# Optimization experiments

Hardware: AMD Instinct MI355X
Metric: run time of the kernel (lower is better)

Reference implementation:

```python
import jax, jax.numpy as jnp
import numpy as np
import math

FILT_LEN = 10  # all Farras / dual filters are 10-tap
INV_SQRT2 = 1.0 / math.sqrt(2.0)

# Farras first-stage analysis filters (fs_farras), shape [tree(2), lo/hi(2), 10]
_F = 0.08838834764832
_G = 0.01122679215254
_H = 0.69587998903400
FAF_NP = np.array([
    [[0.0, -_F, _F, _H, _H, _F, -_F, _G, _G, 0.0],
     [0.0, -_G, _G, _F, _F, -_H, _H, -_F, -_F, 0.0]],
    [[_G, _G, -_F, _F, _H, _H, _F, -_F, 0.0, 0.0],
     [0.0, 0.0, -_F, -_F, _H, -_H, _F, _F, _G, -_G]]], dtype=np.float32)
# Kingsbury Q-shift dual filters (duelfilt / dualfilt1), shape [tree(2), lo/hi(2), 10]
_A = 0.03516384
_B = 0.08832942
_C = 0.23389032
_D = 0.76027237
_E = 0.58751830
_K = 0.11430184
AF_NP = np.array([
    [[_A, 0.0, -_B, _C, _D, _E, 0.0, -_K, 0.0, 0.0],
     [0.0, 0.0, -_K, 0.0, _E, -_D, _C, _B, 0.0, -_A]],
    [[0.0, 0.0, -_K, 0.0, _E, _D, _C, -_B, 0.0, _A],
     [-_A, 0.0, _B, _C, -_D, _E, 0.0, -_K, 0.0, 0.0]]], dtype=np.float32)


def _afb_axis(x, lo_f, hi_f, axis):
    """1D circular analysis filter bank along spatial `axis` (1=rows, 2=cols).
    x: (B,H,W,C). Returns (lo, hi), each halved along `axis`.
    Math: x <- cshift(x,-L); y = downsample2(fullconv(x,f)); wrap-add first L taps.
    """
    N = x.shape[axis]
    L = FILT_LEN // 2
    C = x.shape[-1]
    x = jnp.roll(x, -L, axis=axis)

    def conv(f):
        kf = f[::-1].astype(x.dtype)  # lax does correlation -> flip for convolution
        if axis == 1:
            ker = jnp.tile(kf.reshape(FILT_LEN, 1, 1, 1), (1, 1, 1, C))
            pad = [(FILT_LEN - 1, FILT_LEN - 1), (0, 0)]
            strides = (2, 1)
        else:
            ker = jnp.tile(kf.reshape(1, FILT_LEN, 1, 1), (1, 1, 1, C))
            pad = [(0, 0), (FILT_LEN - 1, FILT_LEN - 1)]
            strides = (1, 2)
        return jax.lax.conv_general_dilated(
            x, ker, window_strides=strides, padding=pad,
            dimension_numbers=('NHWC', 'HWIO', 'NHWC'),
            feature_group_count=C)  # depthwise, per-channel identical filter

    def wrap(y):
        # y has N//2 + L samples along axis; fold periodic tail into head
        head = (jax.lax.slice_in_dim(y, 0, L, axis=axis)
                + jax.lax.slice_in_dim(y, N // 2, N // 2 + L, axis=axis))
        body = jax.lax.slice_in_dim(y, L, N // 2, axis=axis)
        return jnp.concatenate([head, body], axis=axis)

    return wrap(conv(lo_f)), wrap(conv(hi_f))


def afb2d(x, lo_row, hi_row, lo_col, hi_col):
    """2D separable analysis filter bank: returns (lo, [lohi, hilo, hihi])."""
    Lr, Hr = _afb_axis(x, lo_row, hi_row, axis=1)
    lo, w0 = _afb_axis(Lr, lo_col, hi_col, axis=2)
    w1, w2 = _afb_axis(Hr, lo_col, hi_col, axis=2)
    return lo, [w0, w1, w2]


def _add_sub(a, b):
    return (a + b) * INV_SQRT2, (a - b) * INV_SQRT2


def _dtcwt(x, Faf, af, level):
    x = x / 2
    w = [[[None, None] for _ in range(2)] for _ in range(level + 1)]
    for m in range(2):
        for n in range(2):
            lo, w[0][m][n] = afb2d(x, Faf[m, 0], Faf[m, 1], Faf[n, 0], Faf[n, 1])
            for j in range(1, level):
                lo, w[j][m][n] = afb2d(lo, af[m, 0], af[m, 1], af[n, 0], af[n, 1])
            w[level][m][n] = lo
    # combine dual trees into (approx) complex pairs
    for j in range(level):
        for s in range(3):
            w[j][0][0][s], w[j][1][1][s] = _add_sub(w[j][0][0][s], w[j][1][1][s])
            w[j][0][1][s], w[j][1][0][s] = _add_sub(w[j][0][1][s], w[j][1][0][s])
    # multiscale 2x2 tiling reassembly (concat=True path)
    wc = w
    for j in range(level - 1, 0, -1):
        for a in range(2):
            for b in range(2):
                wc[j][a][b] = jnp.concatenate([
                    jnp.concatenate([wc[j + 1][a][b], wc[j][a][b][0]], axis=2),
                    jnp.concatenate([wc[j][a][b][1], wc[j][a][b][2]], axis=2)], axis=1)
    tiles = []
    for a in range(2):
        for b in range(2):
            tiles.append(jnp.concatenate([
                jnp.concatenate([wc[1][a][b], wc[0][a][b][0]], axis=2),
                jnp.concatenate([wc[0][a][b][1], wc[0][a][b][2]], axis=2)], axis=1))
    w0, w1, w2, w3 = tiles
    return jnp.concatenate([jnp.concatenate([w0, w1], axis=2),
                            jnp.concatenate([w2, w3], axis=2)], axis=1)


def setup_inputs() -> dict:
    key = jax.random.key(0)
    x = jax.random.normal(key, (8, 512, 512, 3), dtype=jnp.float32)
    return {"x": x, "Faf": jnp.asarray(FAF_NP), "af": jnp.asarray(AF_NP), "level": 3}


def reference(x, Faf, af, level):
    return _dtcwt(x, Faf, af, int(level))
```

## Files before the change

### kernel.cpp

```cpp
#include <hip/hip_runtime.h>


#define FF 0.08838834764832f
#define GG 0.01122679215254f
#define HHc 0.69587998903400f
#define AAc 0.03516384f
#define BBc 0.08832942f
#define CCc 0.23389032f
#define DDc 0.76027237f
#define EEc 0.58751830f
#define KKc 0.11430184f

__device__ __constant__ float c_filt[2][2][2][10] = {
  {
    { {0.f,-FF, FF, HHc, HHc, FF,-FF, GG, GG, 0.f},
      {0.f,-GG, GG, FF, FF,-HHc, HHc,-FF,-FF, 0.f} },
    { {GG, GG,-FF, FF, HHc, HHc, FF,-FF, 0.f, 0.f},
      {0.f, 0.f,-FF,-FF, HHc,-HHc, FF, FF, GG,-GG} }
  },
  {
    { {AAc, 0.f,-BBc, CCc, DDc, EEc, 0.f,-KKc, 0.f, 0.f},
      {0.f, 0.f,-KKc, 0.f, EEc,-DDc, CCc, BBc, 0.f,-AAc} },
    { {0.f, 0.f,-KKc, 0.f, EEc, DDc, CCc,-BBc, 0.f, AAc},
      {-AAc, 0.f, BBc, CCc,-DDc, EEc, 0.f,-KKc, 0.f, 0.f} }
  }
};

__device__ __forceinline__ void cmb(float& a, float& b) {
  const float k = 0.70710678118654752440f;
  const float s = (a + b) * k, d = (a - b) * k;
  a = s; b = d;
}

__device__ __forceinline__ int swz4(int f4) { return f4 ^ ((f4 >> 3) & 7); }

template<int LVL, int N, int Ho, int Wo, int NT>
__global__ __launch_bounds__(NT) void fused_level(
    const float* __restrict__ src,
    float* __restrict__ llout,
    float* __restrict__ out)
{
  constexpr int half = N / 2;
  constexpr int W2 = 2 * Wo + 8;
  constexpr int NF = (LVL == 0) ? 4 : 8;
  constexpr int ROWF = 3 * N;
  constexpr int FL = 3 * W2;
  constexpr int SIF4 = (3 * W2 * NF) / 4 + 4;
  constexpr size_t ZS = (size_t)8 * N * N * 3;
  constexpr size_t ZOUT = (size_t)8 * half * half * 3;
  static_assert(Ho * Wo * 2 == NT, "stage-B thread map (z-pair split)");
  __shared__ __align__(16) float inter[Ho * SIF4 * 4];

  const int jt = blockIdx.x, it = blockIdx.y, b = blockIdx.z;
  const int i0 = it * Ho, j0 = jt * Wo;
  const int tid = threadIdx.x;

  int base = (2 * j0 - 4) * 3;
  if (base < 0) base += ROWF;

  constexpr int I4 = FL / 4;
  for (int item = tid; item < Ho * I4; item += NT) {
    const int il = item / I4;
    const int q4 = (item - il * I4) * 4;
    int fg = base + q4;
    if (fg >= ROWF) fg -= ROWF;
    const int ig = i0 + il;
    float acc[NF][4];
#pragma unroll
    for (int f = 0; f < NF; ++f)
#pragma unroll
      for (int k = 0; k < 4; ++k) acc[f][k] = 0.f;

    if constexpr (LVL == 0) {
      const float* sp = src + (size_t)b * N * ROWF + fg;
#pragma unroll
      for (int t = 0; t < 10; ++t) {
        const int r = (2 * ig + 5 - t) & (N - 1);
        const float4 v = *(const float4*)(sp + (size_t)r * ROWF);
#pragma unroll
        for (int f = 0; f < 4; ++f) {
          const float fc = c_filt[0][f >> 1][f & 1][t];
          acc[f][0] += fc * v.x; acc[f][1] += fc * v.y;
          acc[f][2] += fc * v.z; acc[f][3] += fc * v.w;
        }
      }
#pragma unroll
      for (int f = 0; f < 4; ++f)
#pragma unroll
        for (int k = 0; k < 4; ++k) acc[f][k] *= 0.5f;
    } else {
#pragma unroll
      for (int z = 0; z < 4; ++z) {
        const int m = z >> 1;
        const float* sp = src + (size_t)z * ZS + (size_t)b * N * ROWF + fg;
#pragma unroll
        for (int t = 0; t < 10; ++t) {
          const int r = (2 * ig + 5 - t) & (N - 1);
          const float4 v = *(const float4*)(sp + (size_t)r * ROWF);
          const float fl = c_filt[1][m][0][t], fh = c_filt[1][m][1][t];
          acc[2 * z][0] += fl * v.x; acc[2 * z][1] += fl * v.y;
          acc[2 * z][2] += fl * v.z; acc[2 * z][3] += fl * v.w;
          acc[2 * z + 1][0] += fh * v.x; acc[2 * z + 1][1] += fh * v.y;
          acc[2 * z + 1][2] += fh * v.z; acc[2 * z + 1][3] += fh * v.w;
        }
      }
    }
#pragma unroll
    for (int k = 0; k < 4; ++k) {
      const int fq = q4 + k;
      if constexpr (NF == 4) {
        float4 w = make_float4(acc[0][k], acc[1][k], acc[2][k], acc[3][k]);
        *(float4*)&inter[(il * SIF4 + swz4(fq)) * 4] = w;
      } else {
        float4 w0 = make_float4(acc[0][k], acc[1][k], acc[2][k], acc[3][k]);
        float4 w1 = make_float4(acc[4][k], acc[5][k], acc[6][k], acc[7][k]);
        *(float4*)&inter[(il * SIF4 + swz4(2 * fq)) * 4] = w0;
        *(float4*)&inter[(il * SIF4 + swz4(2 * fq + 1)) * 4] = w1;
      }
    }
  }
  __syncthreads();

  {
    const int pr = (tid >= Ho * Wo) ? 1 : 0;
    const int t7 = tid - pr * Ho * Wo;
    const int il = t7 / Wo, jl = t7 - (t7 / Wo) * Wo;
    const int za = pr, zb = 3 - pr;
    float LLa[3] = {}, LHa[3] = {}, HLa[3] = {}, HHa[3] = {};
    float LLb[3] = {}, LHb[3] = {}, HLb[3] = {}, HHb[3] = {};
#pragma unroll
    for (int s = 0; s < 10; ++s) {
      const int wl = 2 * jl + 9 - s;
      constexpr int BK = (LVL == 0) ? 0 : 1;
      const float fla = c_filt[BK][pr][0][s],     fha = c_filt[BK][pr][1][s];
      const float flb = c_filt[BK][1 - pr][0][s], fhb = c_filt[BK][1 - pr][1][s];
#pragma unroll
      for (int c = 0; c < 3; ++c) {
        float aa, da, ab, db;
        if constexpr (LVL == 0) {
          const int f4 = wl * 3 + c;
          const float4 v = *(const float4*)&inter[(il * SIF4 + swz4(f4)) * 4];
          aa = v.x; da = v.y; ab = v.z; db = v.w;
        } else {
          const int f4 = (wl * 3 + c) * 2;
          const float4 v0 = *(const float4*)&inter[(il * SIF4 + swz4(f4)) * 4];
          const float4 v1 = *(const float4*)&inter[(il * SIF4 + swz4(f4 + 1)) * 4];
          aa = pr ? v0.z : v0.x; da = pr ? v0.w : v0.y;
          ab = pr ? v1.x : v1.z; db = pr ? v1.y : v1.w;
        }
        LLa[c] += fla * aa; LHa[c] += fha * aa;
        HLa[c] += fla * da; HHa[c] += fha * da;
        LLb[c] += flb * ab; LHb[c] += fhb * ab;
        HLb[c] += flb * db; HHb[c] += fhb * db;
      }
    }
#pragma unroll
    for (int c = 0; c < 3; ++c) {
      cmb(LHa[c], LHb[c]); cmb(HLa[c], HLb[c]); cmb(HHa[c], HHb[c]);
    }
    const int ig = i0 + il, jg = j0 + jl;
    const size_t outB = (size_t)b * (1024u * 1024u * 3u);
    {
      const int m = za >> 1, n = za & 1;
      const int r0 = m * 512, c0 = n * 512;
      float* pLL;
      if constexpr (LVL == 2)
        pLL = out + outB + ((size_t)(r0 + ig) * 1024 + (c0 + jg)) * 3;
      else
        pLL = llout + (size_t)za * ZOUT + (((size_t)b * half + ig) * half + jg) * 3;
      pLL[0] = LLa[0]; pLL[1] = LLa[1]; pLL[2] = LLa[2];
      float* pLH = out + outB + ((size_t)(r0 + ig) * 1024 + (c0 + half + jg)) * 3;
      pLH[0] = LHa[0]; pLH[1] = LHa[1]; pLH[2] = LHa[2];
      float* pHL = out + outB + ((size_t)(r0 + half + ig) * 1024 + (c0 + jg)) * 3;
      pHL[0] = HLa[0]; pHL[1] = HLa[1]; pHL[2] = HLa[2];
      float* pHH = out + outB + ((size_t)(r0 + half + ig) * 1024 + (c0 + half + jg)) * 3;
      pHH[0] = HHa[0]; pHH[1] = HHa[1]; pHH[2] = HHa[2];
    }
    {
      const int m = zb >> 1, n = zb & 1;
      const int r0 = m * 512, c0 = n * 512;
      float* pLL;
      if constexpr (LVL == 2)
        pLL = out + outB + ((size_t)(r0 + ig) * 1024 + (c0 + jg)) * 3;
      else
        pLL = llout + (size_t)zb * ZOUT + (((size_t)b * half + ig) * half + jg) * 3;
      pLL[0] = LLb[0]; pLL[1] = LLb[1]; pLL[2] = LLb[2];
      float* pLH = out + outB + ((size_t)(r0 + ig) * 1024 + (c0 + half + jg)) * 3;
      pLH[0] = LHb[0]; pLH[1] = LHb[1]; pLH[2] = LHb[2];
      float* pHL = out + outB + ((size_t)(r0 + half + ig) * 1024 + (c0 + jg)) * 3;
      pHL[0] = HLb[0]; pHL[1] = HLb[1]; pHL[2] = HLb[2];
      float* pHH = out + outB + ((size_t)(r0 + half + ig) * 1024 + (c0 + half + jg)) * 3;
      pHH[0] = HHb[0]; pHH[1] = HHb[1]; pHH[2] = HHb[2];
    }
  }
}

extern "C" void kernel_launch(void* const* d_in, const int* in_sizes, int n_in,
                              void* d_out, int out_size, void* d_ws, size_t ws_size,
                              hipStream_t stream) {
  (void)in_sizes; (void)n_in; (void)out_size; (void)ws_size;
  const float* x = (const float*)d_in[0];
  float* out = (float*)d_out;
  float* LL1 = (float*)d_ws;
  float* LL2 = LL1 + 6291456;

  fused_level<0, 512, 4, 32, 256><<<dim3(8, 64, 8), 256, 0, stream>>>(x, LL1, out);
  fused_level<1, 256, 8, 16, 256><<<dim3(8, 16, 8), 256, 0, stream>>>(LL1, LL2, out);
  fused_level<2, 128, 4, 16, 128><<<dim3(4, 16, 8), 128, 0, stream>>>(LL2, nullptr, out);
}
```

Measured before the change: 175.3 us.

## Stage level-0 input rows in shared memory and enlarge level-2 tiles

Level 0 gets its own kernel that first loads the block's 2*Ho+8 input rows into shared memory with coalesced float4 loads. The vertical 10-tap filter then reads from LDS, so it no longer issues ten overlapping global row loads per output. The generic kernel drops its level-0 branches, and the level-2 launch moves from 4x16 tiles with 128 threads to 8x16 tiles with 256 threads. The cost is extra shared memory per block at level 0, which may lower occupancy.

```diff
diff --git a/kernel.cpp b/kernel.cpp
--- a/kernel.cpp
+++ b/kernel.cpp
@@ -34,6 +34,130 @@
 
 __device__ __forceinline__ int swz4(int f4) { return f4 ^ ((f4 >> 3) & 7); }
 
+template<int N, int Ho, int Wo, int NT>
+__global__ __launch_bounds__(NT) void fused_level0(
+    const float* __restrict__ src,
+    float* __restrict__ llout,
+    float* __restrict__ out)
+{
+  constexpr int half = N / 2;
+  constexpr int W2 = 2 * Wo + 8;
+  constexpr int ROWF = 3 * N;
+  constexpr int FL = 3 * W2;
+  constexpr int I4 = FL / 4;
+  constexpr int RR = 2 * Ho + 8;
+  constexpr int SIF4 = 3 * W2 + 4;
+  constexpr size_t ZOUT = (size_t)8 * half * half * 3;
+  static_assert(Ho * Wo * 2 == NT, "stage-B thread map (z-pair split)");
+  __shared__ __align__(16) float raw[RR * FL];
+  __shared__ __align__(16) float inter[Ho * SIF4 * 4];
+
+  const int jt = blockIdx.x, it = blockIdx.y, b = blockIdx.z;
+  const int i0 = it * Ho, j0 = jt * Wo;
+  const int tid = threadIdx.x;
+
+  int base = (2 * j0 - 4) * 3;
+  if (base < 0) base += ROWF;
+
+  const float* sb = src + (size_t)b * N * ROWF;
+  for (int item = tid; item < RR * I4; item += NT) {
+    const int lr = item / I4;
+    const int q4 = (item - lr * I4) * 4;
+    int fg = base + q4;
+    if (fg >= ROWF) fg -= ROWF;
+    const int g = (2 * i0 - 4 + lr) & (N - 1);
+    *(float4*)&raw[lr * FL + q4] = *(const float4*)(sb + (size_t)g * ROWF + fg);
+  }
+  __syncthreads();
+
+  for (int item = tid; item < Ho * I4; item += NT) {
+    const int il = item / I4;
+    const int q4 = (item - il * I4) * 4;
+    float acc[4][4];
+#pragma unroll
+    for (int f = 0; f < 4; ++f)
+#pragma unroll
+      for (int k = 0; k < 4; ++k) acc[f][k] = 0.f;
+#pragma unroll
+    for (int t = 0; t < 10; ++t) {
+      const int lr = 2 * il + 9 - t;
+      const float4 v = *(const float4*)&raw[lr * FL + q4];
+#pragma unroll
+      for (int f = 0; f < 4; ++f) {
+        const float fc = c_filt[0][f >> 1][f & 1][t];
+        acc[f][0] += fc * v.x; acc[f][1] += fc * v.y;
+        acc[f][2] += fc * v.z; acc[f][3] += fc * v.w;
+      }
+    }
+#pragma unroll
+    for (int f = 0; f < 4; ++f)
+#pragma unroll
+      for (int k = 0; k < 4; ++k) acc[f][k] *= 0.5f;
+#pragma unroll
+    for (int k = 0; k < 4; ++k) {
+      const int fq = q4 + k;
+      float4 w = make_float4(acc[0][k], acc[1][k], acc[2][k], acc[3][k]);
+      *(float4*)&inter[(il * SIF4 + swz4(fq)) * 4] = w;
+    }
+  }
+  __syncthreads();
+
+  {
+    const int pr = (tid >= Ho * Wo) ? 1 : 0;
+    const int t7 = tid - pr * Ho * Wo;
+    const int il = t7 / Wo, jl = t7 - (t7 / Wo) * Wo;
+    const int za = pr, zb = 3 - pr;
+    float LLa[3] = {}, LHa[3] = {}, HLa[3] = {}, HHa[3] = {};
+    float LLb[3] = {}, LHb[3] = {}, HLb[3] = {}, HHb[3] = {};
+#pragma unroll
+    for (int s = 0; s < 10; ++s) {
+      const int wl = 2 * jl + 9 - s;
+      const float fla = c_filt[0][pr][0][s],     fha = c_filt[0][pr][1][s];
+      const float flb = c_filt[0][1 - pr][0][s], fhb = c_filt[0][1 - pr][1][s];
+#pragma unroll
+      for (int c = 0; c < 3; ++c) {
+        const int f4 = wl * 3 + c;
+        const float4 v = *(const float4*)&inter[(il * SIF4 + swz4(f4)) * 4];
+        const float aa = v.x, da = v.y, ab = v.z, db = v.w;
+        LLa[c] += fla * aa; LHa[c] += fha * aa;
+        HLa[c] += fla * da; HHa[c] += fha * da;
+        LLb[c] += flb * ab; LHb[c] += fhb * ab;
+        HLb[c] += flb * db; HHb[c] += fhb * db;
+      }
+    }
+#pragma unroll
+    for (int c = 0; c < 3; ++c) {
+      cmb(LHa[c], LHb[c]); cmb(HLa[c], HLb[c]); cmb(HHa[c], HHb[c]);
+    }
+    const int ig = i0 + il, jg = j0 + jl;
+    const size_t outB = (size_t)b * (1024u * 1024u * 3u);
+    {
+      const int m = za >> 1, n = za & 1;
+      const int r0 = m * 512, c0 = n * 512;
+      float* pLL = llout + (size_t)za * ZOUT + (((size_t)b * half + ig) * half + jg) * 3;
+      pLL[0] = LLa[0]; pLL[1] = LLa[1]; pLL[2] = LLa[2];
+      float* pLH = out + outB + ((size_t)(r0 + ig) * 1024 + (c0 + half + jg)) * 3;
+      pLH[0] = LHa[0]; pLH[1] = LHa[1]; pLH[2] = LHa[2];
+      float* pHL = out + outB + ((size_t)(r0 + half + ig) * 1024 + (c0 + jg)) * 3;
+      pHL[0] = HLa[0]; pHL[1] = HLa[1]; pHL[2] = HLa[2];
+      float* pHH = out + outB + ((size_t)(r0 + half + ig) * 1024 + (c0 + half + jg)) * 3;
+      pHH[0] = HHa[0]; pHH[1] = HHa[1]; pHH[2] = HHa[2];
+    }
+    {
+      const int m = zb >> 1, n = zb & 1;
+      const int r0 = m * 512, c0 = n * 512;
+      float* pLL = llout + (size_t)zb * ZOUT + (((size_t)b * half + ig) * half + jg) * 3;
+      pLL[0] = LLb[0]; pLL[1] = LLb[1]; pLL[2] = LLb[2];
+      float* pLH = out + outB + ((size_t)(r0 + ig) * 1024 + (c0 + half + jg)) * 3;
+      pLH[0] = LHb[0]; pLH[1] = LHb[1]; pLH[2] = LHb[2];
+      float* pHL = out + outB + ((size_t)(r0 + half + ig) * 1024 + (c0 + jg)) * 3;
+      pHL[0] = HLb[0]; pHL[1] = HLb[1]; pHL[2] = HLb[2];
+      float* pHH = out + outB + ((size_t)(r0 + half + ig) * 1024 + (c0 + half + jg)) * 3;
+      pHH[0] = HHb[0]; pHH[1] = HHb[1]; pHH[2] = HHb[2];
+    }
+  }
+}
+
 template<int LVL, int N, int Ho, int Wo, int NT>
 __global__ __launch_bounds__(NT) void fused_level(
     const float* __restrict__ src,
@@ -42,7 +166,7 @@
 {
   constexpr int half = N / 2;
   constexpr int W2 = 2 * Wo + 8;
-  constexpr int NF = (LVL == 0) ? 4 : 8;
+  constexpr int NF = 8;
   constexpr int ROWF = 3 * N;
   constexpr int FL = 3 * W2;
   constexpr int SIF4 = (3 * W2 * NF) / 4 + 4;
@@ -71,52 +195,28 @@
 #pragma unroll
       for (int k = 0; k < 4; ++k) acc[f][k] = 0.f;
 
-    if constexpr (LVL == 0) {
-      const float* sp = src + (size_t)b * N * ROWF + fg;
+#pragma unroll
+    for (int z = 0; z < 4; ++z) {
+      const int m = z >> 1;
+      const float* sp = src + (size_t)z * ZS + (size_t)b * N * ROWF + fg;
 #pragma unroll
       for (int t = 0; t < 10; ++t) {
         const int r = (2 * ig + 5 - t) & (N - 1);
         const float4 v = *(const float4*)(sp + (size_t)r * ROWF);
-#pragma unroll
-        for (int f = 0; f < 4; ++f) {
-          const float fc = c_filt[0][f >> 1][f & 1][t];
-          acc[f][0] += fc * v.x; acc[f][1] += fc * v.y;
-          acc[f][2] += fc * v.z; acc[f][3] += fc * v.w;
-        }
-      }
-#pragma unroll
-      for (int f = 0; f < 4; ++f)
-#pragma unroll
-        for (int k = 0; k < 4; ++k) acc[f][k] *= 0.5f;
-    } else {
-#pragma unroll
-      for (int z = 0; z < 4; ++z) {
-        const int m = z >> 1;
-        const float* sp = src + (size_t)z * ZS + (size_t)b * N * ROWF + fg;
-#pragma unroll
-        for (int t = 0; t < 10; ++t) {
-          const int r = (2 * ig + 5 - t) & (N - 1);
-          const float4 v = *(const float4*)(sp + (size_t)r * ROWF);
-          const float fl = c_filt[1][m][0][t], fh = c_filt[1][m][1][t];
-          acc[2 * z][0] += fl * v.x; acc[2 * z][1] += fl * v.y;
-          acc[2 * z][2] += fl * v.z; acc[2 * z][3] += fl * v.w;
-          acc[2 * z + 1][0] += fh * v.x; acc[2 * z + 1][1] += fh * v.y;
-          acc[2 * z + 1][2] += fh * v.z; acc[2 * z + 1][3] += fh * v.w;
-        }
+        const float fl = c_filt[1][m][0][t], fh = c_filt[1][m][1][t];
+        acc[2 * z][0] += fl * v.x; acc[2 * z][1] += fl * v.y;
+        acc[2 * z][2] += fl * v.z; acc[2 * z][3] += fl * v.w;
+        acc[2 * z + 1][0] += fh * v.x; acc[2 * z + 1][1] += fh * v.y;
+        acc[2 * z + 1][2] += fh * v.z; acc[2 * z + 1][3] += fh * v.w;
       }
     }
 #pragma unroll
     for (int k = 0; k < 4; ++k) {
       const int fq = q4 + k;
-      if constexpr (NF == 4) {
-        float4 w = make_float4(acc[0][k], acc[1][k], acc[2][k], acc[3][k]);
-        *(float4*)&inter[(il * SIF4 + swz4(fq)) * 4] = w;
-      } else {
-        float4 w0 = make_float4(acc[0][k], acc[1][k], acc[2][k], acc[3][k]);
-        float4 w1 = make_float4(acc[4][k], acc[5][k], acc[6][k], acc[7][k]);
-        *(float4*)&inter[(il * SIF4 + swz4(2 * fq)) * 4] = w0;
-        *(float4*)&inter[(il * SIF4 + swz4(2 * fq + 1)) * 4] = w1;
-      }
+      float4 w0 = make_float4(acc[0][k], acc[1][k], acc[2][k], acc[3][k]);
+      float4 w1 = make_float4(acc[4][k], acc[5][k], acc[6][k], acc[7][k]);
+      *(float4*)&inter[(il * SIF4 + swz4(2 * fq)) * 4] = w0;
+      *(float4*)&inter[(il * SIF4 + swz4(2 * fq + 1)) * 4] = w1;
     }
   }
   __syncthreads();
@@ -131,23 +231,15 @@
 #pragma unroll
     for (int s = 0; s < 10; ++s) {
       const int wl = 2 * jl + 9 - s;
-      constexpr int BK = (LVL == 0) ? 0 : 1;
-      const float fla = c_filt[BK][pr][0][s],     fha = c_filt[BK][pr][1][s];
-      const float flb = c_filt[BK][1 - pr][0][s], fhb = c_filt[BK][1 - pr][1][s];
+      const float fla = c_filt[1][pr][0][s],     fha = c_filt[1][pr][1][s];
+      const float flb = c_filt[1][1 - pr][0][s], fhb = c_filt[1][1 - pr][1][s];
 #pragma unroll
       for (int c = 0; c < 3; ++c) {
-        float aa, da, ab, db;
-        if constexpr (LVL == 0) {
-          const int f4 = wl * 3 + c;
-          const float4 v = *(const float4*)&inter[(il * SIF4 + swz4(f4)) * 4];
-          aa = v.x; da = v.y; ab = v.z; db = v.w;
-        } else {
-          const int f4 = (wl * 3 + c) * 2;
-          const float4 v0 = *(const float4*)&inter[(il * SIF4 + swz4(f4)) * 4];
-          const float4 v1 = *(const float4*)&inter[(il * SIF4 + swz4(f4 + 1)) * 4];
-          aa = pr ? v0.z : v0.x; da = pr ? v0.w : v0.y;
-          ab = pr ? v1.x : v1.z; db = pr ? v1.y : v1.w;
-        }
+        const int f4 = (wl * 3 + c) * 2;
+        const float4 v0 = *(const float4*)&inter[(il * SIF4 + swz4(f4)) * 4];
+        const float4 v1 = *(const float4*)&inter[(il * SIF4 + swz4(f4 + 1)) * 4];
+        const float aa = pr ? v0.z : v0.x, da = pr ? v0.w : v0.y;
+        const float ab = pr ? v1.x : v1.z, db = pr ? v1.y : v1.w;
         LLa[c] += fla * aa; LHa[c] += fha * aa;
         HLa[c] += fla * da; HHa[c] += fha * da;
         LLb[c] += flb * ab; LHb[c] += fhb * ab;
@@ -204,7 +296,7 @@
   float* LL1 = (float*)d_ws;
   float* LL2 = LL1 + 6291456;
 
-  fused_level<0, 512, 4, 32, 256><<<dim3(8, 64, 8), 256, 0, stream>>>(x, LL1, out);
+  fused_level0<512, 4, 32, 256><<<dim3(8, 64, 8), 256, 0, stream>>>(x, LL1, out);
   fused_level<1, 256, 8, 16, 256><<<dim3(8, 16, 8), 256, 0, stream>>>(LL1, LL2, out);
-  fused_level<2, 128, 4, 16, 128><<<dim3(4, 16, 8), 128, 0, stream>>>(LL2, nullptr, out);
+  fused_level<2, 128, 8, 16, 256><<<dim3(4, 8, 8), 256, 0, stream>>>(LL2, nullptr, out);
 }
```

New measurement: 184.9 us. 1.05x slower.
